# Optimization experiments

Hardware: AMD Instinct MI355X
Metric: run time of the kernel (lower is better)

The kernel has to match this reference:

```python
import jax, jax.numpy as jnp
import numpy as np
from jax import lax

TAU = 2.0        # LIFNode default tau, decay_input=True, v_reset=0.0
V_TH = 1.0       # default threshold
SG_ALPHA = 4.0   # surrogate.Sigmoid default alpha
EPS = 1e-5


@jax.custom_vjp
def spike_fn(v):
    return (v >= V_TH).astype(v.dtype)

def _spike_fwd(v):
    return spike_fn(v), v

def _spike_bwd(v, g):
    sg = jax.nn.sigmoid(SG_ALPHA * (v - V_TH))
    return (g * SG_ALPHA * sg * (1.0 - sg),)

spike_fn.defvjp(_spike_fwd, _spike_bwd)


def lif(x_seq):
    """Multi-step LIF: x_seq [T, ...] -> spikes [T, ...]. Hard reset to 0."""
    def step(v, x):
        v = v + (x - v) / TAU          # decay_input integration, v_reset=0
        s = spike_fn(v)
        v = v * (1.0 - s)              # hard reset
        return v, s
    v0 = jnp.zeros_like(x_seq[0])
    _, s_seq = lax.scan(step, v0, x_seq)
    return s_seq


def conv3x3(x, w):
    # x [N,C,H,W], w [O,I,3,3], padding=1, no bias
    return lax.conv_general_dilated(x, w, (1, 1), ((1, 1), (1, 1)),
                                    dimension_numbers=('NCHW', 'OIHW', 'NCHW'))


def tdbn(x, gamma, beta):
    # ThresholdDependentBatchNorm2d: BN over merged (T*B, H, W) per channel
    m = x.mean(axis=(0, 2, 3), keepdims=True)
    v = x.var(axis=(0, 2, 3), keepdims=True)
    return (x - m) * lax.rsqrt(v + EPS) * gamma[None, :, None, None] + beta[None, :, None, None]


def maxpool2(x):
    return lax.reduce_window(x, -jnp.inf, lax.max, (1, 1, 2, 2), (1, 1, 2, 2), 'VALID')


def setup_inputs() -> dict:
    key = jax.random.key(0)
    ks = jax.random.split(key, 5)
    T, B, H, W = 16, 32, 32, 400
    x = jax.random.normal(ks[0], (T, B, 1, H, W), dtype=jnp.float32)
    w1 = jax.random.normal(ks[1], (6, 1, 3, 3), dtype=jnp.float32) * (1.0 / 3.0)
    w2 = jax.random.normal(ks[2], (6, 6, 3, 3), dtype=jnp.float32) * (1.0 / jnp.sqrt(54.0))
    w3 = jax.random.normal(ks[3], (6, 6, 3, 3), dtype=jnp.float32) * (1.0 / jnp.sqrt(54.0))
    kf = jax.random.split(ks[4], 2)
    fw1 = jax.random.normal(kf[0], (100, 1200), dtype=jnp.float32) * (1.0 / jnp.sqrt(1200.0))
    fw2 = jax.random.normal(kf[1], (2, 100), dtype=jnp.float32) * (1.0 / 10.0)
    ones6 = jnp.ones((6,), jnp.float32)
    zeros6 = jnp.zeros((6,), jnp.float32)
    return {"x": x, "w1": w1, "g1": ones6, "b1": zeros6,
            "w2": w2, "g2": ones6, "b2": zeros6,
            "w3": w3, "g3": ones6, "b3": zeros6,
            "fw1": fw1, "fw2": fw2}


def _forward(x, w1, g1, b1, w2, g2, b2, w3, g3, b3, fw1, fw2):
    T, B = x.shape[0], x.shape[1]

    def block(s_seq, w, g, b):
        # conv + tdBN + LIF + maxpool over [T,B,C,H,W]
        TB = s_seq.reshape((T * B,) + s_seq.shape[2:])
        y = tdbn(conv3x3(TB, w), g, b)
        y = y.reshape((T, B) + y.shape[1:])
        s = lif(y)
        p = maxpool2(s.reshape((T * B,) + s.shape[2:]))
        return p.reshape((T, B) + p.shape[1:])

    h = block(x, w1, g1, b1)
    h = block(h, w2, g2, b2)
    h = block(h, w3, g3, b3)          # [T, B, 6, 4, 50]

    h = h.reshape(T, B, -1)            # flatten (C,H,W) -> 1200
    h = lif(jnp.einsum('tbf,of->tbo', h, fw1))   # [T, B, 100]
    out = lif(jnp.einsum('tbf,of->tbo', h, fw2)) # [T, B, 2]
    return out


def reference(x, w1, g1, b1, w2, g2, b2, w3, g3, b3, fw1, fw2):
    return _forward(x, w1, g1, b1, w2, g2, b2, w3, g3, b3, fw1, fw2)
```

## Files before the change

### kernel.cpp

```cpp
#include <hip/hip_runtime.h>


namespace {

constexpr int T = 16, B = 32;
constexpr int H1 = 32, W1 = 400, P1H = 16, P1W = 200;
constexpr int H2 = 16, W2 = 200, P2H = 8,  P2W = 100;
constexpr int H3 = 8,  W3 = 100, P3H = 4,  P3W = 50;

constexpr int NWG_S1 = T * B * (H1 / 32) * (W1 / 100);
constexpr int NWG_F1 = B * (P1H / 4) * (P1W / 10);
constexpr int NWG_F2 = B * (P2H / 4) * (P2W / 5);

constexpr size_t OFF_PART1  = 0;
constexpr size_t OFF_PARTF1 = OFF_PART1 + (size_t)NWG_S1 * 12 * 8;
constexpr size_t OFF_PARTF2 = OFF_PARTF1 + (size_t)6400 * 12 * 8;
constexpr size_t OFF_STATS  = OFF_PARTF2 + (size_t)2560 * 12 * 8;
constexpr size_t OFF_POOL1  = 1310720;
constexpr size_t OFF_POOL2  = OFF_POOL1 + (size_t)T * B * 6 * P1H * P1W * 4;
constexpr size_t OFF_POOL3  = OFF_POOL2 + (size_t)T * B * 6 * P2H * P2W * 4;
constexpr size_t OFF_U1     = OFF_POOL3 + (size_t)T * B * 6 * P3H * P3W * 4;

}

#define LDS_PHASE_BARRIER()                                   \
  do {                                                        \
    asm volatile("s_waitcnt lgkmcnt(0)" ::: "memory");        \
    __builtin_amdgcn_s_barrier();                             \
    __builtin_amdgcn_sched_barrier(0);                        \
  } while (0)

__device__ __forceinline__ float lif_step(float& v, float y) {
  v = v + (y - v) * 0.5f;
  float sp = (v >= 1.0f) ? 1.0f : 0.0f;
  v = (sp > 0.0f) ? 0.0f : v;
  return sp;
}

__device__ __forceinline__ void reduce12(double* s, double* q, double* partials) {
  __shared__ double lds[4][12];
  int lane = threadIdx.x & 63, wid = threadIdx.x >> 6;
#pragma unroll
  for (int k = 0; k < 12; k++) {
    double v = (k < 6) ? s[k] : q[k - 6];
#pragma unroll
    for (int off = 32; off >= 1; off >>= 1) v += __shfl_down(v, off, 64);
    if (lane == 0) lds[wid][k] = v;
  }
  __syncthreads();
  if (threadIdx.x < 12) {
    partials[(size_t)blockIdx.x * 12 + threadIdx.x] =
        lds[0][threadIdx.x] + lds[1][threadIdx.x] + lds[2][threadIdx.x] + lds[3][threadIdx.x];
  }
}

__device__ __forceinline__ void reduce12_sel(int oidx, double s_acc, double q_acc,
                                             double* partials) {
  __shared__ double lds[4][12];
  int lane = threadIdx.x & 63, wid = threadIdx.x >> 6;
#pragma unroll
  for (int k = 0; k < 12; k++) {
    double v = (k == oidx) ? s_acc : ((k == oidx + 6) ? q_acc : 0.0);
#pragma unroll
    for (int off = 32; off >= 1; off >>= 1) v += __shfl_down(v, off, 64);
    if (lane == 0) lds[wid][k] = v;
  }
  __syncthreads();
  if (threadIdx.x < 12) {
    partials[(size_t)blockIdx.x * 12 + threadIdx.x] =
        lds[0][threadIdx.x] + lds[1][threadIdx.x] + lds[2][threadIdx.x] + lds[3][threadIdx.x];
  }
}

template <int NC, int H, int W, int TH, int TW>
__global__ void conv_stats_lds(const float* __restrict__ in, const float* __restrict__ wt,
                               double* __restrict__ partials) {
  constexpr int IH = TH + 2, IW = TW + 2;
  constexpr int IWP = (IW & 1) ? IW : IW + 1;
  constexpr int NW = NC * 54;
  constexpr int NTH = H / TH, NTW = W / TW;
  constexpr int NT = NTH * NTW;
  __shared__ float wsm[NW];
  __shared__ float tile[NC][IH][IWP];

  int tid = threadIdx.x;
  for (int k = tid; k < NW; k += blockDim.x) wsm[k] = wt[k];

  int wg = blockIdx.x;
  int tb = wg / NT;
  int ti = wg % NT;
  int ty = ti / NTW, tx = ti % NTW;
  int h0 = ty * TH - 1, w0 = tx * TW - 1;
  const float* xb = in + (size_t)tb * NC * H * W;

  for (int k = tid; k < NC * IH * IW; k += blockDim.x) {
    int i = k / (IH * IW);
    int r = k % (IH * IW);
    int rr = r / IW, cc = r % IW;
    int hh = h0 + rr, ww = w0 + cc;
    tile[i][rr][cc] = (hh >= 0 && hh < H && ww >= 0 && ww < W) ? xb[i * H * W + hh * W + ww] : 0.0f;
  }
  __syncthreads();

  double s[6] = {0, 0, 0, 0, 0, 0}, q[6] = {0, 0, 0, 0, 0, 0};
  for (int pos = tid; pos < TH * TW; pos += blockDim.x) {
    int ly = pos / TW, lx = pos % TW;
    float acc[6] = {0, 0, 0, 0, 0, 0};
#pragma unroll
    for (int i = 0; i < NC; i++) {
      float p[9];
#pragma unroll
      for (int ky = 0; ky < 3; ky++)
#pragma unroll
        for (int kx = 0; kx < 3; kx++) p[ky * 3 + kx] = tile[i][ly + ky][lx + kx];
#pragma unroll
      for (int o = 0; o < 6; o++) {
        float a = acc[o];
#pragma unroll
        for (int k2 = 0; k2 < 9; k2++) a = fmaf(p[k2], wsm[(o * NC + i) * 9 + k2], a);
        acc[o] = a;
      }
    }
#pragma unroll
    for (int o = 0; o < 6; o++) {
      s[o] += (double)acc[o];
      q[o] += (double)acc[o] * (double)acc[o];
    }
  }
  reduce12(s, q, partials);
}

__global__ void finalize_stats(const double* __restrict__ partials, int nb, double n,
                               const float* __restrict__ gamma,
                               float* __restrict__ mean_out, float* __restrict__ sg_out) {
  __shared__ double lds[12][21];
  __shared__ double sums[12];
  int t = threadIdx.x;
  int k = t % 12, j = t / 12;
  if (t < 252) {
    double acc = 0.0;
    for (int b = j; b < nb; b += 21) acc += partials[(size_t)b * 12 + k];
    lds[k][j] = acc;
  }
  __syncthreads();
  if (t < 12) {
    double acc = 0.0;
#pragma unroll
    for (int j2 = 0; j2 < 21; j2++) acc += lds[t][j2];
    sums[t] = acc;
  }
  __syncthreads();
  if (t < 6) {
    double mean = sums[t] / n;
    double var = sums[t + 6] / n - mean * mean;
    double invstd = 1.0 / sqrt(var + 1e-5);
    mean_out[t] = (float)mean;
    sg_out[t] = (float)(invstd * (double)gamma[t]);
  }
}

__global__ void fuse1_stats(const float* __restrict__ x, const float* __restrict__ w1g,
                            const float* __restrict__ w2g,
                            const float* __restrict__ mean1, const float* __restrict__ sg1,
                            const float* __restrict__ beta1,
                            float* __restrict__ pool1, double* __restrict__ partials2) {
  __shared__ float wsm1[54];
  __shared__ float wsm2[324];
  __shared__ float til[2][14][13];
  __shared__ float phl[474];
  __shared__ float pr[40][7][7];

  int tid = threadIdx.x;
  for (int k = tid; k < 54; k += 256) wsm1[k] = w1g[k];
  for (int k = tid; k < 324; k += 256) wsm2[k] = w2g[k];

  int wg = blockIdx.x;
  int b = wg / 80;
  int rem = wg % 80;
  int oy = rem / 20, ox = rem % 20;
  int iy0 = 8 * oy - 3, ix0 = 20 * ox - 3;

  bool s_in[2];
  int s_off[2], s_lofs[2];
#pragma unroll
  for (int j = 0; j < 2; j++) {
    int k = tid + 256 * j;
    bool valid = k < 364;
    int srr = k / 26, scc = k % 26;
    int shh = iy0 + srr, sww = ix0 + scc;
    s_in[j] = valid && shh >= 0 && shh < H1 && sww >= 0 && sww < W1;
    s_off[j] = shh * W1 + sww;
    s_lofs[j] = valid ? ((scc & 1) * 182 + srr * 13 + (scc >> 1)) : -1;
  }
  float* tilf = &til[0][0][0];

  int hch[2], hhy[2], hhx[2], hpy[2], hpx[2], hphl[2];
  bool hact[2], hval[2], hown[2];
  float m_[2], sc_[2], be_[2];
  float wv[2][9];
#pragma unroll
  for (int sl = 0; sl < 2; sl++) {
    int pos = tid + 256 * sl;
    hact[sl] = pos < 432;
    int p2 = hact[sl] ? pos : 0;
    int ch = p2 / 72;
    int r = p2 % 72;
    int hy = r / 12, hx = r % 12;
    hch[sl] = ch; hhy[sl] = hy; hhx[sl] = hx;
    hphl[sl] = ch * 79 + hy * 13 + hx;
    int py = 4 * oy - 1 + hy, px = 10 * ox - 1 + hx;
    hpy[sl] = py; hpx[sl] = px;
    hval[sl] = hact[sl] && py >= 0 && py < P1H && px >= 0 && px < P1W;
    hown[sl] = hact[sl] && hy >= 1 && hy <= 4 && hx >= 1 && hx <= 10;
#pragma unroll
    for (int k = 0; k < 9; k++) wv[sl][k] = w1g[ch * 9 + k];
    m_[sl] = mean1[ch]; sc_[sl] = sg1[ch]; be_[sl] = beta1[ch];
  }

  int oidx = (tid < 240) ? (tid / 40) : -1;
  int pos40 = tid % 40;
  int psy = pos40 / 10, psx = pos40 % 10;

  float v[2][4];
#pragma unroll
  for (int sl = 0; sl < 2; sl++)
#pragma unroll
    for (int k = 0; k < 4; k++) v[sl][k] = 0.0f;
  double s_acc = 0.0, q_acc = 0.0;

  float rs[2] = {0.0f, 0.0f};
#pragma unroll
  for (int j = 0; j < 2; j++)
    if (s_in[j]) rs[j] = x[(size_t)(0 * B + b) * (H1 * W1) + s_off[j]];

  for (int t = 0; t < T; t++) {
    __syncthreads();
#pragma unroll
    for (int j = 0; j < 2; j++)
      if (s_lofs[j] >= 0) tilf[s_lofs[j]] = rs[j];
    if (t + 1 < T) {
#pragma unroll
      for (int j = 0; j < 2; j++)
        if (s_in[j]) rs[j] = x[(size_t)((t + 1) * B + b) * (H1 * W1) + s_off[j]];
    }
    LDS_PHASE_BARRIER();
#pragma unroll
    for (int sl = 0; sl < 2; sl++) {
      if (hact[sl]) {
        float smax = 0.0f;
        if (hval[sl]) {
          int ry = 2 * hhy[sl], hx = hhx[sl];
          float p[16];
#pragma unroll
          for (int r = 0; r < 4; r++) {
            p[r * 4 + 0] = til[0][ry + r][hx];
            p[r * 4 + 1] = til[1][ry + r][hx];
            p[r * 4 + 2] = til[0][ry + r][hx + 1];
            p[r * 4 + 3] = til[1][ry + r][hx + 1];
          }
#pragma unroll
          for (int dy = 0; dy < 2; dy++) {
#pragma unroll
            for (int dx = 0; dx < 2; dx++) {
              float acc = 0.0f;
#pragma unroll
              for (int ky = 0; ky < 3; ky++)
#pragma unroll
                for (int kx = 0; kx < 3; kx++)
                  acc = fmaf(p[(dy + ky) * 4 + dx + kx], wv[sl][ky * 3 + kx], acc);
              float y = (acc - m_[sl]) * sc_[sl] + be_[sl];
              float sp = lif_step(v[sl][dy * 2 + dx], y);
              smax = fmaxf(smax, sp);
            }
          }
        }
        phl[hphl[sl]] = smax;
        if (hown[sl])
          pool1[((size_t)(t * B + b) * 6 + hch[sl]) * (P1H * P1W) + hpy[sl] * P1W + hpx[sl]] = smax;
      }
    }
    LDS_PHASE_BARRIER();
    if (oidx >= 0) {
      int i2 = oidx;
      float pt[9];
#pragma unroll
      for (int ky = 0; ky < 3; ky++)
#pragma unroll
        for (int kx = 0; kx < 3; kx++)
          pt[ky * 3 + kx] = phl[i2 * 79 + (psy + ky) * 13 + (psx + kx)];
      float p6[6];
#pragma unroll
      for (int o = 0; o < 6; o++) {
        float a = 0.0f;
#pragma unroll
        for (int k2 = 0; k2 < 9; k2++) a = fmaf(pt[k2], wsm2[(o * 6 + i2) * 9 + k2], a);
        p6[o] = a;
      }
#pragma unroll
      for (int o = 0; o < 6; o++) pr[pos40][i2][o] = p6[o];
    }
    LDS_PHASE_BARRIER();
    if (oidx >= 0) {
      double acc = 0.0;
#pragma unroll
      for (int ic = 0; ic < 6; ic++) acc += (double)pr[pos40][ic][oidx];
      s_acc += acc;
      q_acc += acc * acc;
    }
  }
  __syncthreads();
  reduce12_sel(oidx, s_acc, q_acc, partials2);
}

__global__ void fuse2_stats(const float* __restrict__ in, const float* __restrict__ w2g,
                            const float* __restrict__ w3g,
                            const float* __restrict__ mean2, const float* __restrict__ sg2,
                            const float* __restrict__ beta2,
                            float* __restrict__ pool2, double* __restrict__ partials3) {
  __shared__ float wsm2[324];
  __shared__ float wsm3[324];
  __shared__ float til[2][6][14][9];
  __shared__ float phl[6][6][7];
  __shared__ float pr[20][6][7];

  int tid = threadIdx.x;
  for (int k = tid; k < 324; k += 256) { wsm2[k] = w2g[k]; wsm3[k] = w3g[k]; }

  int wg = blockIdx.x;
  int b = wg / 40;
  int rem = wg % 40;
  int oy = rem / 20, ox = rem % 20;
  int iy0 = 8 * oy - 3, ix0 = 10 * ox - 3;
  constexpr int HW = H2 * W2;

  bool s_in[6];
  int s_off[6], s_lofs[6];
#pragma unroll
  for (int j = 0; j < 6; j++) {
    int k = tid + 256 * j;
    bool valid = k < 1344;
    int i = k / 224;
    int r2 = k % 224;
    int rr = r2 / 16, cc = r2 % 16;
    int hh = iy0 + rr, ww = ix0 + cc;
    s_in[j] = valid && hh >= 0 && hh < H2 && ww >= 0 && ww < W2;
    s_off[j] = i * HW + hh * W2 + ww;
    s_lofs[j] = valid ? ((cc & 1) * 756 + i * 126 + rr * 9 + (cc >> 1)) : -1;
  }
  float* tilf = &til[0][0][0][0];

  bool active = tid < 252;
  int ch = 0, hy = 0, hx = 0, py = 0, px = 0;
  bool pvalid = false, own = false;
  if (active) {
    ch = tid / 42;
    int r = tid % 42;
    hy = r / 7; hx = r % 7;
    py = 4 * oy - 1 + hy; px = 5 * ox - 1 + hx;
    pvalid = (py >= 0 && py < P2H && px >= 0 && px < P2W);
    own = (hy >= 1 && hy <= 4 && hx >= 1 && hx <= 5);
  }
  float m = active ? mean2[ch] : 0.0f;
  float sc = active ? sg2[ch] : 0.0f;
  float be = active ? beta2[ch] : 0.0f;

  bool ppact = tid < 240;
  int pg = tid / 20;
  int ppos = tid % 20;
  int pi2 = pg % 6;
  int pob = (pg / 6) * 3;
  int ppsy = ppos / 5, ppsx = ppos % 5;

  int oidx = (tid < 120) ? (tid / 20) : -1;
  int pos = tid % 20;

  float v[4] = {0.0f, 0.0f, 0.0f, 0.0f};
  double s_acc = 0.0, q_acc = 0.0;

  float rs[6] = {0.0f, 0.0f, 0.0f, 0.0f, 0.0f, 0.0f};
  {
    const float* xb = in + (size_t)(0 * B + b) * 6 * HW;
#pragma unroll
    for (int j = 0; j < 6; j++)
      if (s_in[j]) rs[j] = xb[s_off[j]];
  }

  for (int t = 0; t < T; t++) {
    __syncthreads();
#pragma unroll
    for (int j = 0; j < 6; j++)
      if (s_lofs[j] >= 0) tilf[s_lofs[j]] = rs[j];
    if (t + 1 < T) {
      const float* xb = in + (size_t)((t + 1) * B + b) * 6 * HW;
#pragma unroll
      for (int j = 0; j < 6; j++)
        if (s_in[j]) rs[j] = xb[s_off[j]];
    }
    LDS_PHASE_BARRIER();
    if (active) {
      float smax = 0.0f;
      if (pvalid) {
        int ry = 2 * hy;
        float acc4[4] = {0.0f, 0.0f, 0.0f, 0.0f};
#pragma unroll
        for (int i = 0; i < 6; i++) {
          float p[16];
#pragma unroll
          for (int r = 0; r < 4; r++) {
            p[r * 4 + 0] = til[0][i][ry + r][hx];
            p[r * 4 + 1] = til[1][i][ry + r][hx];
            p[r * 4 + 2] = til[0][i][ry + r][hx + 1];
            p[r * 4 + 3] = til[1][i][ry + r][hx + 1];
          }
          const float* wo = &wsm2[(ch * 6 + i) * 9];
#pragma unroll
          for (int dy = 0; dy < 2; dy++)
#pragma unroll
            for (int dx = 0; dx < 2; dx++) {
              float a = acc4[dy * 2 + dx];
#pragma unroll
              for (int ky = 0; ky < 3; ky++)
#pragma unroll
                for (int kx = 0; kx < 3; kx++)
                  a = fmaf(p[(dy + ky) * 4 + dx + kx], wo[ky * 3 + kx], a);
              acc4[dy * 2 + dx] = a;
            }
        }
#pragma unroll
        for (int p4 = 0; p4 < 4; p4++) {
          float y = (acc4[p4] - m) * sc + be;
          float sp = lif_step(v[p4], y);
          smax = fmaxf(smax, sp);
        }
      }
      phl[ch][hy][hx] = smax;
      if (own)
        pool2[((size_t)(t * B + b) * 6 + ch) * (P2H * P2W) + py * P2W + px] = smax;
    }
    LDS_PHASE_BARRIER();
    if (ppact) {
      float pt[9];
#pragma unroll
      for (int ky = 0; ky < 3; ky++)
#pragma unroll
        for (int kx = 0; kx < 3; kx++)
          pt[ky * 3 + kx] = phl[pi2][ppsy + ky][ppsx + kx];
#pragma unroll
      for (int oo = 0; oo < 3; oo++) {
        int o = pob + oo;
        float a = 0.0f;
#pragma unroll
        for (int k2 = 0; k2 < 9; k2++) a = fmaf(pt[k2], wsm3[(o * 6 + pi2) * 9 + k2], a);
        pr[ppos][pi2][o] = a;
      }
    }
    LDS_PHASE_BARRIER();
    if (oidx >= 0) {
      double acc = 0.0;
#pragma unroll
      for (int ic = 0; ic < 6; ic++) acc += (double)pr[pos][ic][oidx];
      s_acc += acc;
      q_acc += acc * acc;
    }
  }
  __syncthreads();
  reduce12_sel(oidx, s_acc, q_acc, partials3);
}

template <int H, int W, int PH, int PW, int TH, int TW>
__global__ void block6_fuse_lds(const float* __restrict__ in, const float* __restrict__ wt,
                                const float* __restrict__ mean, const float* __restrict__ sg,
                                const float* __restrict__ beta, float* __restrict__ out) {
  constexpr int NTH = PH / TH, NTW = PW / TW;
  constexpr int IH = 2 * TH + 2, IW = 2 * TW + 2;
  constexpr int EW = IW / 2;
  constexpr int TILE_N = IH * IW;
  constexpr int NACT = 6 * TH * TW;
  constexpr int HW = H * W;
  __shared__ float wsm[324];
  __shared__ float til_e[6][IH][EW];
  __shared__ float til_o[6][IH][EW];

  for (int k = threadIdx.x; k < 324; k += blockDim.x) wsm[k] = wt[k];

  int wg = blockIdx.x;
  int b = wg / (NTH * NTW);
  int tid2 = wg % (NTH * NTW);
  int ty = tid2 / NTW, tx = tid2 % NTW;
  int h_in0 = 2 * (ty * TH) - 1, w_in0 = 2 * (tx * TW) - 1;

  int tid = threadIdx.x;
  int o = 0, lph = 0, lpw = 0;
  if (tid < NACT) {
    o = tid / (TH * TW);
    int r = tid % (TH * TW);
    lph = r / TW; lpw = r % TW;
  }
  float m = mean[o], s = sg[o], be = beta[o];
  float v[4] = {0.0f, 0.0f, 0.0f, 0.0f};

  for (int t = 0; t < T; t++) {
    __syncthreads();
    const float* xb = in + (size_t)(t * B + b) * 6 * HW;
    for (int k = tid; k < 6 * TILE_N; k += blockDim.x) {
      int i = k / TILE_N;
      int r2 = k % TILE_N;
      int rr = r2 / IW, cc = r2 % IW;
      int hh = h_in0 + rr, ww = w_in0 + cc;
      float val = (hh >= 0 && hh < H && ww >= 0 && ww < W) ? xb[i * HW + hh * W + ww] : 0.0f;
      if (cc & 1) til_o[i][rr][cc >> 1] = val;
      else        til_e[i][rr][cc >> 1] = val;
    }
    __syncthreads();
    if (tid < NACT) {
      int ry = 2 * lph;
      float acc[4] = {0.0f, 0.0f, 0.0f, 0.0f};
#pragma unroll
      for (int i = 0; i < 6; i++) {
        float p[16];
#pragma unroll
        for (int r = 0; r < 4; r++) {
          p[r * 4 + 0] = til_e[i][ry + r][lpw];
          p[r * 4 + 1] = til_o[i][ry + r][lpw];
          p[r * 4 + 2] = til_e[i][ry + r][lpw + 1];
          p[r * 4 + 3] = til_o[i][ry + r][lpw + 1];
        }
        const float* wo = &wsm[(o * 6 + i) * 9];
#pragma unroll
        for (int dy = 0; dy < 2; dy++)
#pragma unroll
          for (int dx = 0; dx < 2; dx++) {
            float a = acc[dy * 2 + dx];
#pragma unroll
            for (int ky = 0; ky < 3; ky++)
#pragma unroll
              for (int kx = 0; kx < 3; kx++)
                a = fmaf(p[(dy + ky) * 4 + dx + kx], wo[ky * 3 + kx], a);
            acc[dy * 2 + dx] = a;
          }
      }
      float smax = 0.0f;
#pragma unroll
      for (int p4 = 0; p4 < 4; p4++) {
        float y = (acc[p4] - m) * s + be;
        float sp = lif_step(v[p4], y);
        smax = fmaxf(smax, sp);
      }
      out[((size_t)(t * B + b) * 6 + o) * (PH * PW) + (ty * TH + lph) * PW + (tx * TW + lpw)] = smax;
    }
  }
}

__global__ void fc1_mm(const float* __restrict__ p3, const float* __restrict__ fw1,
                       float* __restrict__ u1) {
  int idx = blockIdx.x * blockDim.x + threadIdx.x;
  if (idx >= T * B * 100) return;
  int o = idx % 100;
  int tb = idx / 100;
  const float4* x4 = (const float4*)(p3 + (size_t)tb * 1200);
  const float4* w4 = (const float4*)(fw1 + (size_t)o * 1200);
  float acc = 0.0f;
#pragma unroll 4
  for (int k = 0; k < 300; k++) {
    float4 a = x4[k], w = w4[k];
    acc = fmaf(a.x, w.x, acc);
    acc = fmaf(a.y, w.y, acc);
    acc = fmaf(a.z, w.z, acc);
    acc = fmaf(a.w, w.w, acc);
  }
  u1[idx] = acc;
}

__global__ void fc_tail(const float* __restrict__ u1, const float* __restrict__ fw2,
                        float* __restrict__ outp) {
  __shared__ float s1[100];
  __shared__ float w2s[200];
  int b = blockIdx.x;
  int tid = threadIdx.x;
  for (int k = tid; k < 200; k += 128) w2s[k] = fw2[k];
  float v1 = 0.0f, v2 = 0.0f;
  __syncthreads();
  for (int t = 0; t < T; t++) {
    if (tid < 100) {
      float sp = lif_step(v1, u1[(size_t)(t * B + b) * 100 + tid]);
      s1[tid] = sp;
    }
    __syncthreads();
    if (tid < 2) {
      const float* wr = &w2s[tid * 100];
      float acc = 0.0f;
#pragma unroll
      for (int k = 0; k < 100; k++) acc = fmaf(s1[k], wr[k], acc);
      float sp = lif_step(v2, acc);
      outp[(size_t)(t * B + b) * 2 + tid] = sp;
    }
    __syncthreads();
  }
}

extern "C" void kernel_launch(void* const* d_in, const int* in_sizes, int n_in,
                              void* d_out, int out_size, void* d_ws, size_t ws_size,
                              hipStream_t stream) {
  const float* x   = (const float*)d_in[0];
  const float* w1  = (const float*)d_in[1];
  const float* g1  = (const float*)d_in[2];
  const float* b1  = (const float*)d_in[3];
  const float* w2  = (const float*)d_in[4];
  const float* g2  = (const float*)d_in[5];
  const float* b2  = (const float*)d_in[6];
  const float* w3  = (const float*)d_in[7];
  const float* g3  = (const float*)d_in[8];
  const float* b3  = (const float*)d_in[9];
  const float* fw1 = (const float*)d_in[10];
  const float* fw2 = (const float*)d_in[11];
  float* out = (float*)d_out;

  char* ws = (char*)d_ws;
  double* part1  = (double*)(ws + OFF_PART1);
  double* partf1 = (double*)(ws + OFF_PARTF1);
  double* partf2 = (double*)(ws + OFF_PARTF2);
  float* mean1 = (float*)(ws + OFF_STATS + 0);
  float* sg1   = (float*)(ws + OFF_STATS + 32);
  float* mean2 = (float*)(ws + OFF_STATS + 64);
  float* sg2   = (float*)(ws + OFF_STATS + 96);
  float* mean3 = (float*)(ws + OFF_STATS + 128);
  float* sg3   = (float*)(ws + OFF_STATS + 160);
  float* pool1 = (float*)(ws + OFF_POOL1);
  float* pool2 = (float*)(ws + OFF_POOL2);
  float* pool3 = (float*)(ws + OFF_POOL3);
  float* u1    = (float*)(ws + OFF_U1);

  conv_stats_lds<1, H1, W1, 32, 100><<<NWG_S1, 256, 0, stream>>>(x, w1, part1);
  finalize_stats<<<1, 256, 0, stream>>>(part1, NWG_S1, (double)T * B * H1 * W1, g1, mean1, sg1);
  fuse1_stats<<<NWG_F1, 256, 0, stream>>>(x, w1, w2, mean1, sg1, b1, pool1, partf1);
  finalize_stats<<<1, 256, 0, stream>>>(partf1, NWG_F1, (double)T * B * H2 * W2, g2, mean2, sg2);
  fuse2_stats<<<NWG_F2, 256, 0, stream>>>(pool1, w2, w3, mean2, sg2, b2, pool2, partf2);
  finalize_stats<<<1, 256, 0, stream>>>(partf2, NWG_F2, (double)T * B * H3 * W3, g3, mean3, sg3);
  {
    int nwg = B * (P3H / 2) * (P3W / 5);
    block6_fuse_lds<H3, W3, P3H, P3W, 2, 5><<<nwg, 64, 0, stream>>>(pool2, w3, mean3, sg3, b3, pool3);
  }
  {
    int n = T * B * 100;
    fc1_mm<<<(n + 255) / 256, 256, 0, stream>>>(pool3, fw1, u1);
  }
  fc_tail<<<B, 128, 0, stream>>>(u1, fw2, out);
}
```

Before: 434.7 us.

## Process two timesteps per iteration in fuse1_stats to halve barriers

The fuse1_stats loop over time now handles two timesteps per iteration. It double-sizes the input tile, pooled-spike and partial-sum LDS buffers and prefetches two frames of input at once. This halves the number of block-wide barriers and loop iterations, giving more independent work between synchronisations. In exchange it uses more LDS and registers, which could reduce occupancy.

```diff
diff --git a/kernel.cpp b/kernel.cpp
--- a/kernel.cpp
+++ b/kernel.cpp
@@ -166,9 +166,9 @@
                             float* __restrict__ pool1, double* __restrict__ partials2) {
   __shared__ float wsm1[54];
   __shared__ float wsm2[324];
-  __shared__ float til[2][14][13];
-  __shared__ float phl[474];
-  __shared__ float pr[40][7][7];
+  __shared__ float til[2][2][14][13];
+  __shared__ float phl[2][474];
+  __shared__ float pr[2][40][49];
 
   int tid = threadIdx.x;
   for (int k = tid; k < 54; k += 256) wsm1[k] = w1g[k];
@@ -180,19 +180,22 @@
   int oy = rem / 20, ox = rem % 20;
   int iy0 = 8 * oy - 3, ix0 = 20 * ox - 3;
 
-  bool s_in[2];
-  int s_off[2], s_lofs[2];
-#pragma unroll
-  for (int j = 0; j < 2; j++) {
+  bool s_in[3];
+  int s_sp[3], s_lofs[3], s_tt[3];
+#pragma unroll
+  for (int j = 0; j < 3; j++) {
     int k = tid + 256 * j;
-    bool valid = k < 364;
-    int srr = k / 26, scc = k % 26;
+    bool valid = k < 728;
+    int tt = k / 364;
+    int r = k % 364;
+    int srr = r / 26, scc = r % 26;
     int shh = iy0 + srr, sww = ix0 + scc;
     s_in[j] = valid && shh >= 0 && shh < H1 && sww >= 0 && sww < W1;
-    s_off[j] = shh * W1 + sww;
-    s_lofs[j] = valid ? ((scc & 1) * 182 + srr * 13 + (scc >> 1)) : -1;
-  }
-  float* tilf = &til[0][0][0];
+    s_sp[j] = shh * W1 + sww;
+    s_tt[j] = tt;
+    s_lofs[j] = valid ? (tt * 364 + (scc & 1) * 182 + srr * 13 + (scc >> 1)) : -1;
+  }
+  float* tilf = &til[0][0][0][0];
 
   int hch[2], hhy[2], hhx[2], hpy[2], hpx[2], hphl[2];
   bool hact[2], hval[2], hown[2];
@@ -228,84 +231,91 @@
     for (int k = 0; k < 4; k++) v[sl][k] = 0.0f;
   double s_acc = 0.0, q_acc = 0.0;
 
-  float rs[2] = {0.0f, 0.0f};
-#pragma unroll
-  for (int j = 0; j < 2; j++)
-    if (s_in[j]) rs[j] = x[(size_t)(0 * B + b) * (H1 * W1) + s_off[j]];
-
-  for (int t = 0; t < T; t++) {
+  float rs[3] = {0.0f, 0.0f, 0.0f};
+#pragma unroll
+  for (int j = 0; j < 3; j++)
+    if (s_in[j]) rs[j] = x[(size_t)(s_tt[j] * B + b) * (H1 * W1) + s_sp[j]];
+
+  for (int t = 0; t < T; t += 2) {
     __syncthreads();
 #pragma unroll
-    for (int j = 0; j < 2; j++)
+    for (int j = 0; j < 3; j++)
       if (s_lofs[j] >= 0) tilf[s_lofs[j]] = rs[j];
-    if (t + 1 < T) {
-#pragma unroll
-      for (int j = 0; j < 2; j++)
-        if (s_in[j]) rs[j] = x[(size_t)((t + 1) * B + b) * (H1 * W1) + s_off[j]];
+    if (t + 2 < T) {
+#pragma unroll
+      for (int j = 0; j < 3; j++)
+        if (s_in[j]) rs[j] = x[(size_t)((t + 2 + s_tt[j]) * B + b) * (H1 * W1) + s_sp[j]];
     }
     LDS_PHASE_BARRIER();
 #pragma unroll
     for (int sl = 0; sl < 2; sl++) {
       if (hact[sl]) {
-        float smax = 0.0f;
-        if (hval[sl]) {
-          int ry = 2 * hhy[sl], hx = hhx[sl];
-          float p[16];
-#pragma unroll
-          for (int r = 0; r < 4; r++) {
-            p[r * 4 + 0] = til[0][ry + r][hx];
-            p[r * 4 + 1] = til[1][ry + r][hx];
-            p[r * 4 + 2] = til[0][ry + r][hx + 1];
-            p[r * 4 + 3] = til[1][ry + r][hx + 1];
-          }
-#pragma unroll
-          for (int dy = 0; dy < 2; dy++) {
-#pragma unroll
-            for (int dx = 0; dx < 2; dx++) {
-              float acc = 0.0f;
-#pragma unroll
-              for (int ky = 0; ky < 3; ky++)
-#pragma unroll
-                for (int kx = 0; kx < 3; kx++)
-                  acc = fmaf(p[(dy + ky) * 4 + dx + kx], wv[sl][ky * 3 + kx], acc);
-              float y = (acc - m_[sl]) * sc_[sl] + be_[sl];
-              float sp = lif_step(v[sl][dy * 2 + dx], y);
-              smax = fmaxf(smax, sp);
+#pragma unroll
+        for (int tt = 0; tt < 2; tt++) {
+          float smax = 0.0f;
+          if (hval[sl]) {
+            int ry = 2 * hhy[sl], hx = hhx[sl];
+            float p[16];
+#pragma unroll
+            for (int r = 0; r < 4; r++) {
+              p[r * 4 + 0] = til[tt][0][ry + r][hx];
+              p[r * 4 + 1] = til[tt][1][ry + r][hx];
+              p[r * 4 + 2] = til[tt][0][ry + r][hx + 1];
+              p[r * 4 + 3] = til[tt][1][ry + r][hx + 1];
+            }
+#pragma unroll
+            for (int dy = 0; dy < 2; dy++) {
+#pragma unroll
+              for (int dx = 0; dx < 2; dx++) {
+                float acc = 0.0f;
+#pragma unroll
+                for (int ky = 0; ky < 3; ky++)
+#pragma unroll
+                  for (int kx = 0; kx < 3; kx++)
+                    acc = fmaf(p[(dy + ky) * 4 + dx + kx], wv[sl][ky * 3 + kx], acc);
+                float y = (acc - m_[sl]) * sc_[sl] + be_[sl];
+                float sp = lif_step(v[sl][dy * 2 + dx], y);
+                smax = fmaxf(smax, sp);
+              }
             }
           }
+          phl[tt][hphl[sl]] = smax;
+          if (hown[sl])
+            pool1[((size_t)((t + tt) * B + b) * 6 + hch[sl]) * (P1H * P1W) +
+                  hpy[sl] * P1W + hpx[sl]] = smax;
         }
-        phl[hphl[sl]] = smax;
-        if (hown[sl])
-          pool1[((size_t)(t * B + b) * 6 + hch[sl]) * (P1H * P1W) + hpy[sl] * P1W + hpx[sl]] = smax;
       }
     }
     LDS_PHASE_BARRIER();
     if (oidx >= 0) {
       int i2 = oidx;
-      float pt[9];
-#pragma unroll
-      for (int ky = 0; ky < 3; ky++)
-#pragma unroll
-        for (int kx = 0; kx < 3; kx++)
-          pt[ky * 3 + kx] = phl[i2 * 79 + (psy + ky) * 13 + (psx + kx)];
-      float p6[6];
-#pragma unroll
-      for (int o = 0; o < 6; o++) {
-        float a = 0.0f;
-#pragma unroll
-        for (int k2 = 0; k2 < 9; k2++) a = fmaf(pt[k2], wsm2[(o * 6 + i2) * 9 + k2], a);
-        p6[o] = a;
-      }
-#pragma unroll
-      for (int o = 0; o < 6; o++) pr[pos40][i2][o] = p6[o];
+#pragma unroll
+      for (int tt = 0; tt < 2; tt++) {
+        float pt[9];
+#pragma unroll
+        for (int ky = 0; ky < 3; ky++)
+#pragma unroll
+          for (int kx = 0; kx < 3; kx++)
+            pt[ky * 3 + kx] = phl[tt][i2 * 79 + (psy + ky) * 13 + (psx + kx)];
+#pragma unroll
+        for (int o = 0; o < 6; o++) {
+          float a = 0.0f;
+#pragma unroll
+          for (int k2 = 0; k2 < 9; k2++) a = fmaf(pt[k2], wsm2[(o * 6 + i2) * 9 + k2], a);
+          pr[tt][pos40][i2 * 7 + o] = a;
+        }
+      }
     }
     LDS_PHASE_BARRIER();
     if (oidx >= 0) {
-      double acc = 0.0;
-#pragma unroll
-      for (int ic = 0; ic < 6; ic++) acc += (double)pr[pos40][ic][oidx];
-      s_acc += acc;
-      q_acc += acc * acc;
+#pragma unroll
+      for (int tt = 0; tt < 2; tt++) {
+        double acc = 0.0;
+#pragma unroll
+        for (int ic = 0; ic < 6; ic++) acc += (double)pr[tt][pos40][ic * 7 + oidx];
+        s_acc += acc;
+        q_acc += acc * acc;
+      }
     }
   }
   __syncthreads();
```

After: 479.1 us. 10.2% more time.
